# Optimization experiments

Hardware: AMD Instinct MI355X
Metric: run time of the kernel (lower is better)

Reference implementation:

```python
import jax, jax.numpy as jnp
import numpy as np

L_LAYERS = 4
B = 8
PATCH_H = 37
PATCH_W = 37
P = PATCH_H * PATCH_W  # 1369
D = 1024
J = 768
H = 518
W = 518
R_LIST = [1, 3, 5]
K_LIST = [1, 2, 3]
TOPMIN_MIN = 0.0
TOPMIN_MAX = 0.3


def setup_inputs() -> dict:
    key = jax.random.key(0)
    k1, k2 = jax.random.split(key)
    features = jax.random.normal(k1, (L_LAYERS, B, P, D), dtype=jnp.float32)
    cls_tokens = jax.random.normal(k2, (B, J), dtype=jnp.float32)
    return {"features": features, "cls_tokens": cls_tokens}


def _layer_norm_2d(x, eps=1e-5):
    # torch.layer_norm with normalized_shape = (P, D): normalize jointly over last two dims, no affine
    mu = jnp.mean(x, axis=(-2, -1), keepdims=True)
    var = jnp.var(x, axis=(-2, -1), keepdims=True)
    return (x - mu) * jax.lax.rsqrt(var + eps)


def _lnamd(features, r):
    # LNAMD: unfold(r,r, zero pad r//2) + adaptive_avg_pool1d(D*r*r -> D) == per-channel r x r
    # neighborhood mean over the patch grid with zero padding (pool bins are exactly r*r wide).
    if r == 1:
        return features
    l, b, p, d = features.shape
    x = features.reshape(l * b, PATCH_H, PATCH_W, d)
    pad = r // 2
    s = jax.lax.reduce_window(x, 0.0, jax.lax.add, (1, r, r, 1), (1, 1, 1, 1),
                              [(0, 0), (pad, pad), (pad, pad), (0, 0)])
    return (s / float(r * r)).reshape(l, b, p, d)


def _msm(rf, use_remat=False):
    # rf: [L,B,P,D] L2-normalized. Mutual scoring: for each image i, euclidean cdist of its
    # patches to all other images' patches, min over ref patches, mean of [k_min:k_max] smallest.
    l, b, p, d = rf.shape
    k_min = int(TOPMIN_MIN * (b - 1))
    k_max = int(TOPMIN_MAX * (b - 1))
    sq = jnp.sum(rf * rf, axis=-1)  # [L,B,P]

    def per_image(i):
        feat = rf[:, i]  # [L,P,D]
        dots = jnp.einsum('lpd,lbqd->lpbq', feat, rf)  # [L,P,B,P]
        d2 = sq[:, i][:, :, None, None] + sq[:, None, :, :] - 2.0 * dots
        dist = jnp.sqrt(jnp.maximum(d2, 1e-12))
        mind = jnp.min(dist, axis=-1)  # [L,P,B]
        mind = jnp.where(jnp.arange(b)[None, None, :] == i, jnp.inf, mind)  # exclude self
        neg_top = jax.lax.top_k(-mind, k_max)[0]  # k_max smallest distances (ascending)
        sel = -neg_top[..., k_min:k_max]
        return jnp.mean(sel, axis=-1)  # [L,P]

    fn = jax.checkpoint(per_image) if use_remat else per_image
    scores = jax.lax.map(fn, jnp.arange(b))  # [B,L,P]; lax.map keeps one cdist block live at a time
    return jnp.transpose(scores, (1, 0, 2))  # [L,B,P]


def _rscin(sim, scores, top_k):
    # zero out the B-top_k smallest similarities per row (keep top_k largest), row-normalize, reweight
    b = sim.shape[0]
    if top_k < b:
        vals, idx = jax.lax.top_k(sim, top_k)
        masked = jnp.zeros_like(sim).at[jnp.arange(b)[:, None], idx].set(vals)
    else:
        masked = sim
    masked = masked / jnp.sum(masked, axis=-1, keepdims=True)
    return masked @ scores


def _interp_mat(out_len, in_len):
    # bilinear, align_corners=True: src = dst * (in-1)/(out-1); separable 1D interpolation matrix
    pos = jnp.arange(out_len, dtype=jnp.float32) * ((in_len - 1) / (out_len - 1))
    i0 = jnp.clip(jnp.floor(pos).astype(jnp.int32), 0, in_len - 1)
    i1 = jnp.minimum(i0 + 1, in_len - 1)
    w = pos - i0.astype(jnp.float32)
    m = jnp.zeros((out_len, in_len), jnp.float32)
    m = m.at[jnp.arange(out_len), i0].add(1.0 - w)
    m = m.at[jnp.arange(out_len), i1].add(w)
    return m


def _forward(features, cls_tokens, use_remat=False):
    feats = _layer_norm_2d(features)  # [L,B,P,D]
    per_r = []
    for r in R_LIST:
        rf = _lnamd(feats, r)
        rf = rf / jnp.linalg.norm(rf, axis=-1, keepdims=True)
        per_r.append(jnp.mean(_msm(rf, use_remat), axis=0))  # mean over layers -> [B,P]
    scores = jnp.mean(jnp.stack(per_r, axis=0), axis=0)  # [B,P]
    img_scores = jnp.max(scores, axis=1)  # [B]
    cls = cls_tokens / jnp.linalg.norm(cls_tokens, axis=-1, keepdims=True)
    sim = cls @ cls.T  # [B,B]
    final = jnp.mean(jnp.stack([_rscin(sim, img_scores, k) for k in K_LIST], axis=0), axis=0)
    patch = scores.reshape(-1, PATCH_H, PATCH_W)
    mh = _interp_mat(H, PATCH_H)
    mw = _interp_mat(W, PATCH_W)
    pixel = jnp.einsum('Hh,bhw,Ww->bHW', mh, patch, mw)  # [B,H,W]
    return final, pixel


def reference(features, cls_tokens):
    return _forward(features, cls_tokens)
```

## Files before the change

### kernel.cpp

```cpp
#include <hip/hip_runtime.h>
#include <hip/hip_bf16.h>
#include <math.h>

#define L_LAYERS 4
#define BIMG 8
#define PATCH_H 37
#define PATCH_W 37
#define PP 1369
#define DD 1024
#define JJ 768
#define HOUT 518
#define WOUT 518
#define PPAD 1408
#define NPAIR 28

typedef float floatx4 __attribute__((ext_vector_type(4)));

__device__ __forceinline__ unsigned int f2e4m3(float v) {
  unsigned int b = __float_as_uint(v);
  unsigned int sign = (b >> 24) & 0x80u;
  float mag = fabsf(v);
  unsigned int code;
  if (mag >= 0.015625f) {
    unsigned int mb = __float_as_uint(mag);
    mb = mb + 0x0007ffffu + ((mb >> 20) & 1u);
    code = (((mb >> 23) - 120u) << 3) | ((mb >> 20) & 7u);
  } else {
    code = (unsigned int)__float2int_rn(mag * 512.0f);
  }
  return code | sign;
}
__device__ __forceinline__ float e4m3tof(unsigned int c) {
  unsigned int em = c & 0x7fu;
  float m;
  if (em >= 8u) m = __uint_as_float((((em >> 3) + 120u) << 23) | ((em & 7u) << 20));
  else          m = (float)em * 0.001953125f;
  return (c & 0x80u) ? -m : m;
}

__device__ __forceinline__ void gload_lds16(const void* gptr, void* lptr) {
  __builtin_amdgcn_global_load_lds(
      (const __attribute__((address_space(1))) unsigned int*)gptr,
      (__attribute__((address_space(3))) unsigned int*)lptr, 16, 0, 0);
}

__global__ __launch_bounds__(256) void k1_mu(const float* __restrict__ x,
                                             float* __restrict__ mu_acc) {
  const int lb = blockIdx.y;
  const float* base = x + (size_t)lb * PP * DD;
  const int N4 = PP * DD / 4;
  float s = 0.0f;
  for (int idx = blockIdx.x * 256 + threadIdx.x; idx < N4; idx += gridDim.x * 256) {
    float4 u = *(const float4*)(base + (size_t)idx * 4);
    s += u.x + u.y + u.z + u.w;
  }
  for (int off = 1; off < 64; off <<= 1) s += __shfl_xor(s, off, 64);
  __shared__ float red[4];
  if ((threadIdx.x & 63) == 0) red[threadIdx.x >> 6] = s;
  __syncthreads();
  if (threadIdx.x == 0)
    atomicAdd(&mu_acc[lb], red[0] + red[1] + red[2] + red[3]);
}

__global__ __launch_bounds__(256) void k2_pool(const float* __restrict__ x,
                                               const float* __restrict__ mu_acc,
                                               unsigned char* __restrict__ rf,
                                               float* __restrict__ nrm,
                                               int r) {
  const int p  = blockIdx.x;
  const int lb = blockIdx.y;
  const int tid = threadIdx.x;
  const int d0 = tid * 4;
  const size_t outbase = ((size_t)lb * PPAD + p) * DD;
  if (p >= PP) {
    uchar4 z; z.x = 0; z.y = 0; z.z = 0; z.w = 0;
    *(uchar4*)(rf + outbase + d0) = z;
    if (tid == 0) nrm[(size_t)lb * PPAD + p] = 0.0f;
    return;
  }
  const float mu = mu_acc[lb] * (1.0f / ((float)PP * (float)DD));
  const int ph = p / PATCH_W, pw = p % PATCH_W;
  const int pad = r >> 1;
  float s0 = 0, s1 = 0, s2 = 0, s3 = 0;
  int cnt = 0;
  for (int dy = -pad; dy <= pad; dy++) {
    int qh = ph + dy; if (qh < 0 || qh >= PATCH_H) continue;
    for (int dx = -pad; dx <= pad; dx++) {
      int qw = pw + dx; if (qw < 0 || qw >= PATCH_W) continue;
      cnt++;
      const float* src = x + ((size_t)lb * PP + qh * PATCH_W + qw) * DD + d0;
      float4 u = *(const float4*)src;
      s0 += u.x; s1 += u.y; s2 += u.z; s3 += u.w;
    }
  }
  const float cm = (float)cnt * mu;
  s0 -= cm; s1 -= cm; s2 -= cm; s3 -= cm;
  float sq = s0 * s0 + s1 * s1 + s2 * s2 + s3 * s3;
  for (int off = 1; off < 64; off <<= 1) sq += __shfl_xor(sq, off, 64);
  __shared__ float red[4];
  if ((tid & 63) == 0) red[tid >> 6] = sq;
  __syncthreads();
  const float rn16 = rsqrtf(red[0] + red[1] + red[2] + red[3]) * 16.0f;
  unsigned int c0 = f2e4m3(s0 * rn16), c1 = f2e4m3(s1 * rn16);
  unsigned int c2 = f2e4m3(s2 * rn16), c3 = f2e4m3(s3 * rn16);
  uchar4 o; o.x = (unsigned char)c0; o.y = (unsigned char)c1;
  o.z = (unsigned char)c2; o.w = (unsigned char)c3;
  *(uchar4*)(rf + outbase + d0) = o;
  float q0 = e4m3tof(c0), q1 = e4m3tof(c1), q2 = e4m3tof(c2), q3 = e4m3tof(c3);
  float nq = q0 * q0 + q1 * q1 + q2 * q2 + q3 * q3;
  for (int off = 1; off < 64; off <<= 1) nq += __shfl_xor(nq, off, 64);
  __syncthreads();
  if ((tid & 63) == 0) red[tid >> 6] = nq;
  __syncthreads();
  if (tid == 0)
    nrm[(size_t)lb * PPAD + p] = red[0] + red[1] + red[2] + red[3];
}

__global__ __launch_bounds__(256) void k3_pairdots(const unsigned char* __restrict__ rf,
                                                   const float* __restrict__ nrm,
                                                   unsigned int* __restrict__ mind) {
  const int l = blockIdx.z / NPAIR;
  int rem = blockIdx.z % NPAIR;
  int i = 0, span = BIMG - 1;
  while (rem >= span) { rem -= span; span--; i++; }
  const int j = i + 1 + rem;

  const int rowbase = blockIdx.x * 128;
  const int colbase = blockIdx.y * 128;
  const unsigned char* A  = rf + ((size_t)(l * BIMG + i) * PPAD + rowbase) * DD;
  const unsigned char* Bp = rf + ((size_t)(l * BIMG + j) * PPAD + colbase) * DD;

  __shared__ __align__(16) unsigned char lA[128 * 64];
  __shared__ __align__(16) unsigned char lB[128 * 64];

  const int tid  = threadIdx.x;
  const int lane = tid & 63;
  const int wave = tid >> 6;
  const int lrow = lane & 15;
  const int quad = lane >> 4;
  const int wr = (wave >> 1) * 64;
  const int wc = (wave & 1) * 64;

  floatx4 acc[4][4];
#pragma unroll
  for (int a = 0; a < 4; a++)
#pragma unroll
    for (int b = 0; b < 4; b++) acc[a][b] = (floatx4){0.f, 0.f, 0.f, 0.f};

  const int r0  = wave * 32 + (lane >> 2);
  const int gsw = (lane & 3) ^ ((lane >> 3) & 3);
  const unsigned char* gA0 = A  + (size_t)r0 * DD + gsw * 16;
  const unsigned char* gA1 = gA0 + (size_t)16 * DD;
  const unsigned char* gB0 = Bp + (size_t)r0 * DD + gsw * 16;
  const unsigned char* gB1 = gB0 + (size_t)16 * DD;
  unsigned char* dA0 = lA + wave * 2048;
  unsigned char* dA1 = dA0 + 1024;
  unsigned char* dB0 = lB + wave * 2048;
  unsigned char* dB1 = dB0 + 1024;

  const int swf = (lrow >> 1) & 3;
  const int sub8 = (quad & 1) * 8;
  int rowoffA[4], rowoffB[4];
#pragma unroll
  for (int t = 0; t < 4; t++) {
    rowoffA[t] = (wr + t * 16 + lrow) * 64 + sub8;
    rowoffB[t] = (wc + t * 16 + lrow) * 64 + sub8;
  }

  for (int k0 = 0; k0 < DD; k0 += 64) {
    __syncthreads();
    gload_lds16(gA0 + k0, dA0);
    gload_lds16(gA1 + k0, dA1);
    gload_lds16(gB0 + k0, dB0);
    gload_lds16(gB1 + k0, dB1);
    __syncthreads();
#pragma unroll
    for (int ks = 0; ks < 2; ks++) {
      const int gfrag = (((ks << 1) + (quad >> 1)) ^ swf) * 16;
      long af[4], bfv[4];
#pragma unroll
      for (int mt = 0; mt < 4; mt++)
        af[mt] = *(const long*)(lA + rowoffA[mt] + gfrag);
#pragma unroll
      for (int ct = 0; ct < 4; ct++)
        bfv[ct] = *(const long*)(lB + rowoffB[ct] + gfrag);
#pragma unroll
      for (int mt = 0; mt < 4; mt++)
#pragma unroll
        for (int ct = 0; ct < 4; ct++)
          acc[mt][ct] = __builtin_amdgcn_mfma_f32_16x16x32_fp8_fp8(
              af[mt], bfv[ct], acc[mt][ct], 0, 0, 0);
    }
  }

  const float* nI = nrm + (size_t)(l * BIMG + i) * PPAD;
  const float* nJ = nrm + (size_t)(l * BIMG + j) * PPAD;
  unsigned int* mrow = mind + ((size_t)(l * BIMG + i) * BIMG + j) * PP;
  unsigned int* mcol = mind + ((size_t)(l * BIMG + j) * BIMG + i) * PP;

  float nj[4];
#pragma unroll
  for (int ct = 0; ct < 4; ct++) nj[ct] = nJ[colbase + wc + ct * 16 + lrow];
  float ni[4][4];
#pragma unroll
  for (int mt = 0; mt < 4; mt++)
#pragma unroll
    for (int reg = 0; reg < 4; reg++)
      ni[mt][reg] = nI[rowbase + wr + mt * 16 + quad * 4 + reg];

#pragma unroll
  for (int mt = 0; mt < 4; mt++) {
#pragma unroll
    for (int reg = 0; reg < 4; reg++) {
      const int gr = rowbase + wr + mt * 16 + quad * 4 + reg;
      float v = -1e30f;
#pragma unroll
      for (int ct = 0; ct < 4; ct++) {
        const int gc = colbase + wc + ct * 16 + lrow;
        if (gc < PP) v = fmaxf(v, 2.0f * acc[mt][ct][reg] - nj[ct]);
      }
      for (int off = 1; off < 16; off <<= 1) v = fmaxf(v, __shfl_xor(v, off, 64));
      if (lrow == 0 && gr < PP)
        atomicMax(mrow + gr, __float_as_uint(v + 1024.0f));
    }
  }
#pragma unroll
  for (int ct = 0; ct < 4; ct++) {
    const int gc = colbase + wc + ct * 16 + lrow;
    float v = -1e30f;
#pragma unroll
    for (int mt = 0; mt < 4; mt++) {
      const int grb = rowbase + wr + mt * 16 + quad * 4;
#pragma unroll
      for (int reg = 0; reg < 4; reg++)
        if (grb + reg < PP) v = fmaxf(v, 2.0f * acc[mt][ct][reg] - ni[mt][reg]);
    }
    for (int off = 16; off < 64; off <<= 1) v = fmaxf(v, __shfl_xor(v, off, 64));
    if (quad == 0 && gc < PP)
      atomicMax(mcol + gc, __float_as_uint(v + 1024.0f));
  }
}

__global__ void k4_scores(const unsigned int* __restrict__ mind,
                          const float* __restrict__ nrm,
                          float* __restrict__ scores) {
  const int idx = blockIdx.x * 256 + threadIdx.x;
  if (idx >= BIMG * PP) return;
  const int i = idx / PP, p = idx % PP;
  float accum = 0.0f;
  for (int l = 0; l < L_LAYERS; l++) {
    const float n_own = nrm[(size_t)(l * BIMG + i) * PPAD + p];
    float m1 = 1e30f, m2 = 1e30f;
    for (int b = 0; b < BIMG; b++) {
      if (b == i) continue;
      const unsigned int enc = mind[((size_t)(l * BIMG + i) * BIMG + b) * PP + p];
      const float val = __uint_as_float(enc) - 1024.0f;
      const float d2 = fmaxf((n_own - val) * (1.0f / 256.0f), 1e-12f);
      const float dist = sqrtf(d2);
      if (dist < m1) { m2 = m1; m1 = dist; }
      else if (dist < m2) { m2 = dist; }
    }
    accum += 0.5f * (m1 + m2);
  }
  scores[idx] += accum * (1.0f / (float)(L_LAYERS * 3));
}

__global__ void k5_imgmax(const float* __restrict__ scores, float* __restrict__ img) {
  const int i = blockIdx.x;
  float m = -1e30f;
  for (int p = threadIdx.x; p < PP; p += 256) m = fmaxf(m, scores[i * PP + p]);
  for (int off = 1; off < 64; off <<= 1) m = fmaxf(m, __shfl_xor(m, off, 64));
  __shared__ float red[4];
  if ((threadIdx.x & 63) == 0) red[threadIdx.x >> 6] = m;
  __syncthreads();
  if (threadIdx.x == 0)
    img[i] = fmaxf(fmaxf(red[0], red[1]), fmaxf(red[2], red[3]));
}

__global__ void k6_final(const float* __restrict__ cls,
                         const float* __restrict__ img,
                         float* __restrict__ out) {
  __shared__ float norms[BIMG];
  __shared__ float sim[BIMG][BIMG];
  const int t = threadIdx.x;
  if (t < BIMG) {
    float s = 0;
    for (int d = 0; d < JJ; d++) { float v = cls[t * JJ + d]; s += v * v; }
    norms[t] = sqrtf(s);
  }
  __syncthreads();
  {
    const int ii = t >> 3, jj = t & 7;
    float s = 0;
    for (int d = 0; d < JJ; d++) s += cls[ii * JJ + d] * cls[jj * JJ + d];
    sim[ii][jj] = s / (norms[ii] * norms[jj]);
  }
  __syncthreads();
  if (t < BIMG) {
    float v[8]; int id[8];
    for (int a = 0; a < 8; a++) { v[a] = sim[t][a]; id[a] = a; }
    for (int a = 0; a < 8; a++) {
      int best = a;
      for (int b = a + 1; b < 8; b++) if (v[b] > v[best]) best = b;
      float tv = v[a]; v[a] = v[best]; v[best] = tv;
      int ti = id[a]; id[a] = id[best]; id[best] = ti;
    }
    float res = 0;
    for (int k = 1; k <= 3; k++) {
      float num = 0, den = 0;
      for (int a = 0; a < k; a++) { num += v[a] * img[id[a]]; den += v[a]; }
      res += num / den;
    }
    out[t] = res * (1.0f / 3.0f);
  }
}

__global__ void k7_pixel(const float* __restrict__ scores,
                         float* __restrict__ out) {
  const int idx = blockIdx.x * 256 + threadIdx.x;
  if (idx >= BIMG * HOUT * WOUT) return;
  const int b = idx / (HOUT * WOUT);
  const int rem = idx % (HOUT * WOUT);
  const int Y = rem / WOUT, X = rem % WOUT;
  const float sy = (float)(PATCH_H - 1) / (float)(HOUT - 1);
  const float sx = (float)(PATCH_W - 1) / (float)(WOUT - 1);
  float py = (float)Y * sy;
  float px = (float)X * sx;
  int y0 = (int)floorf(py); y0 = min(max(y0, 0), PATCH_H - 1);
  int x0 = (int)floorf(px); x0 = min(max(x0, 0), PATCH_W - 1);
  const int y1 = min(y0 + 1, PATCH_H - 1);
  const int x1 = min(x0 + 1, PATCH_W - 1);
  const float wy = py - (float)y0, wx = px - (float)x0;
  const float* sc = scores + (size_t)b * PP;
  const float v =
      (1.f - wy) * ((1.f - wx) * sc[y0 * PATCH_W + x0] + wx * sc[y0 * PATCH_W + x1]) +
      wy         * ((1.f - wx) * sc[y1 * PATCH_W + x0] + wx * sc[y1 * PATCH_W + x1]);
  out[8 + idx] = v;
}

extern "C" void kernel_launch(void* const* d_in, const int* in_sizes, int n_in,
                              void* d_out, int out_size, void* d_ws, size_t ws_size,
                              hipStream_t stream) {
  const float* feat = (const float*)d_in[0];
  const float* cls  = (const float*)d_in[1];
  float* out = (float*)d_out;

  char* ws = (char*)d_ws;
  size_t off = 0;
  unsigned char* rf = (unsigned char*)(ws + off);
  off += (size_t)L_LAYERS * BIMG * PPAD * DD;
  unsigned int* mind = (unsigned int*)(ws + off);
  off += (size_t)L_LAYERS * BIMG * BIMG * PP * 4;
  float* nrm = (float*)(ws + off);
  off += (size_t)L_LAYERS * BIMG * PPAD * 4;
  float* scores = (float*)(ws + off);
  off += (size_t)BIMG * PP * 4;
  float* mu_acc = (float*)(ws + off);
  off += 32 * 4;
  float* img = (float*)(ws + off);
  off += 8 * 4;

  hipMemsetAsync(mu_acc, 0, 32 * 4, stream);
  hipMemsetAsync(scores, 0, (size_t)BIMG * PP * 4, stream);
  k1_mu<<<dim3(43, 32), 256, 0, stream>>>(feat, mu_acc);

  const int rlist[3] = {1, 3, 5};
  for (int ri = 0; ri < 3; ri++) {
    k2_pool<<<dim3(PPAD, 32), 256, 0, stream>>>(feat, mu_acc, rf, nrm, rlist[ri]);
    hipMemsetAsync(mind, 0, (size_t)L_LAYERS * BIMG * BIMG * PP * 4, stream);
    k3_pairdots<<<dim3(11, 11, L_LAYERS * NPAIR), 256, 0, stream>>>(rf, nrm, mind);
    k4_scores<<<(BIMG * PP + 255) / 256, 256, 0, stream>>>(mind, nrm, scores);
  }
  k5_imgmax<<<8, 256, 0, stream>>>(scores, img);
  k6_final<<<1, 64, 0, stream>>>(cls, img, out);
  k7_pixel<<<(BIMG * HOUT * WOUT + 255) / 256, 256, 0, stream>>>(scores, out);
}
```

Before: 2.594 ms.

## Fuse all three pooling radii into single pool, pairdots and score launches

Adds a k2_pool3 kernel that reads each 5x5 neighborhood once and produces the r=1, r=3 and r=5 FP8 features and norms together. The pair-dot GEMM and score kernels then run once over all three radii via a larger grid, in place of three sequential rounds of launches. A launch_bounds occupancy hint is added to k3, and its precomputed norm and offset arrays are replaced by direct loads to lower register use. This cuts feature reads and launch serialization and gives k3 a bigger grid, at the cost of three times the workspace; it falls back to the old path if the workspace is too small.

```diff
diff --git a/kernel.cpp b/kernel.cpp
--- a/kernel.cpp
+++ b/kernel.cpp
@@ -13,6 +13,10 @@
 #define WOUT 518
 #define PPAD 1408
 #define NPAIR 28
+#define ZPAIR (L_LAYERS * NPAIR)
+#define RFSZ  ((size_t)L_LAYERS * BIMG * PPAD * DD)
+#define NRMSZ ((size_t)L_LAYERS * BIMG * PPAD)
+#define MINDSZ ((size_t)L_LAYERS * BIMG * BIMG * PP)
 
 typedef float floatx4 __attribute__((ext_vector_type(4)));
 
@@ -62,19 +66,85 @@
     atomicAdd(&mu_acc[lb], red[0] + red[1] + red[2] + red[3]);
 }
 
-__global__ __launch_bounds__(256) void k2_pool(const float* __restrict__ x,
-                                               const float* __restrict__ mu_acc,
-                                               unsigned char* __restrict__ rf,
-                                               float* __restrict__ nrm,
-                                               int r) {
+__device__ __forceinline__ void finish_r(float s0, float s1, float s2, float s3,
+                                         float cm, unsigned char* dst, float* nrmdst,
+                                         int tid, float* red) {
+  s0 -= cm; s1 -= cm; s2 -= cm; s3 -= cm;
+  float sq = s0 * s0 + s1 * s1 + s2 * s2 + s3 * s3;
+  for (int off = 1; off < 64; off <<= 1) sq += __shfl_xor(sq, off, 64);
+  __syncthreads();
+  if ((tid & 63) == 0) red[tid >> 6] = sq;
+  __syncthreads();
+  const float rn16 = rsqrtf(red[0] + red[1] + red[2] + red[3]) * 16.0f;
+  unsigned int c0 = f2e4m3(s0 * rn16), c1 = f2e4m3(s1 * rn16);
+  unsigned int c2 = f2e4m3(s2 * rn16), c3 = f2e4m3(s3 * rn16);
+  uchar4 o; o.x = (unsigned char)c0; o.y = (unsigned char)c1;
+  o.z = (unsigned char)c2; o.w = (unsigned char)c3;
+  *(uchar4*)dst = o;
+  float q0 = e4m3tof(c0), q1 = e4m3tof(c1), q2 = e4m3tof(c2), q3 = e4m3tof(c3);
+  float nq = q0 * q0 + q1 * q1 + q2 * q2 + q3 * q3;
+  for (int off = 1; off < 64; off <<= 1) nq += __shfl_xor(nq, off, 64);
+  __syncthreads();
+  if ((tid & 63) == 0) red[tid >> 6] = nq;
+  __syncthreads();
+  if (tid == 0) *nrmdst = red[0] + red[1] + red[2] + red[3];
+}
+
+__global__ __launch_bounds__(256) void k2_pool3(const float* __restrict__ x,
+                                                const float* __restrict__ mu_acc,
+                                                unsigned char* __restrict__ rf,
+                                                float* __restrict__ nrm) {
   const int p  = blockIdx.x;
   const int lb = blockIdx.y;
   const int tid = threadIdx.x;
   const int d0 = tid * 4;
-  const size_t outbase = ((size_t)lb * PPAD + p) * DD;
+  const size_t outoff = ((size_t)lb * PPAD + p) * DD + d0;
   if (p >= PP) {
     uchar4 z; z.x = 0; z.y = 0; z.z = 0; z.w = 0;
-    *(uchar4*)(rf + outbase + d0) = z;
+    for (int r = 0; r < 3; r++) {
+      *(uchar4*)(rf + r * RFSZ + outoff) = z;
+      if (tid == 0) nrm[r * NRMSZ + (size_t)lb * PPAD + p] = 0.0f;
+    }
+    return;
+  }
+  const float mu = mu_acc[lb] * (1.0f / ((float)PP * (float)DD));
+  const int ph = p / PATCH_W, pw = p % PATCH_W;
+  float a5[4] = {0, 0, 0, 0}, a3[4] = {0, 0, 0, 0}, a1[4] = {0, 0, 0, 0};
+  int c5 = 0, c3 = 0;
+  for (int dy = -2; dy <= 2; dy++) {
+    int qh = ph + dy; if (qh < 0 || qh >= PATCH_H) continue;
+    for (int dx = -2; dx <= 2; dx++) {
+      int qw = pw + dx; if (qw < 0 || qw >= PATCH_W) continue;
+      const float* src = x + ((size_t)lb * PP + qh * PATCH_W + qw) * DD + d0;
+      float4 u = *(const float4*)src;
+      a5[0] += u.x; a5[1] += u.y; a5[2] += u.z; a5[3] += u.w; c5++;
+      if (dy >= -1 && dy <= 1 && dx >= -1 && dx <= 1) {
+        a3[0] += u.x; a3[1] += u.y; a3[2] += u.z; a3[3] += u.w; c3++;
+        if (dy == 0 && dx == 0) { a1[0] = u.x; a1[1] = u.y; a1[2] = u.z; a1[3] = u.w; }
+      }
+    }
+  }
+  __shared__ float red[4];
+  const size_t noff = (size_t)lb * PPAD + p;
+  finish_r(a1[0], a1[1], a1[2], a1[3], mu, rf + outoff, nrm + noff, tid, red);
+  finish_r(a3[0], a3[1], a3[2], a3[3], (float)c3 * mu, rf + RFSZ + outoff,
+           nrm + NRMSZ + noff, tid, red);
+  finish_r(a5[0], a5[1], a5[2], a5[3], (float)c5 * mu, rf + 2 * RFSZ + outoff,
+           nrm + 2 * NRMSZ + noff, tid, red);
+}
+
+__global__ __launch_bounds__(256) void k2_pool(const float* __restrict__ x,
+                                               const float* __restrict__ mu_acc,
+                                               unsigned char* __restrict__ rf,
+                                               float* __restrict__ nrm, int r) {
+  const int p  = blockIdx.x;
+  const int lb = blockIdx.y;
+  const int tid = threadIdx.x;
+  const int d0 = tid * 4;
+  const size_t outoff = ((size_t)lb * PPAD + p) * DD + d0;
+  if (p >= PP) {
+    uchar4 z; z.x = 0; z.y = 0; z.z = 0; z.w = 0;
+    *(uchar4*)(rf + outoff) = z;
     if (tid == 0) nrm[(size_t)lb * PPAD + p] = 0.0f;
     return;
   }
@@ -93,42 +163,27 @@
       s0 += u.x; s1 += u.y; s2 += u.z; s3 += u.w;
     }
   }
-  const float cm = (float)cnt * mu;
-  s0 -= cm; s1 -= cm; s2 -= cm; s3 -= cm;
-  float sq = s0 * s0 + s1 * s1 + s2 * s2 + s3 * s3;
-  for (int off = 1; off < 64; off <<= 1) sq += __shfl_xor(sq, off, 64);
   __shared__ float red[4];
-  if ((tid & 63) == 0) red[tid >> 6] = sq;
-  __syncthreads();
-  const float rn16 = rsqrtf(red[0] + red[1] + red[2] + red[3]) * 16.0f;
-  unsigned int c0 = f2e4m3(s0 * rn16), c1 = f2e4m3(s1 * rn16);
-  unsigned int c2 = f2e4m3(s2 * rn16), c3 = f2e4m3(s3 * rn16);
-  uchar4 o; o.x = (unsigned char)c0; o.y = (unsigned char)c1;
-  o.z = (unsigned char)c2; o.w = (unsigned char)c3;
-  *(uchar4*)(rf + outbase + d0) = o;
-  float q0 = e4m3tof(c0), q1 = e4m3tof(c1), q2 = e4m3tof(c2), q3 = e4m3tof(c3);
-  float nq = q0 * q0 + q1 * q1 + q2 * q2 + q3 * q3;
-  for (int off = 1; off < 64; off <<= 1) nq += __shfl_xor(nq, off, 64);
-  __syncthreads();
-  if ((tid & 63) == 0) red[tid >> 6] = nq;
-  __syncthreads();
-  if (tid == 0)
-    nrm[(size_t)lb * PPAD + p] = red[0] + red[1] + red[2] + red[3];
-}
-
-__global__ __launch_bounds__(256) void k3_pairdots(const unsigned char* __restrict__ rf,
-                                                   const float* __restrict__ nrm,
-                                                   unsigned int* __restrict__ mind) {
-  const int l = blockIdx.z / NPAIR;
-  int rem = blockIdx.z % NPAIR;
+  finish_r(s0, s1, s2, s3, (float)cnt * mu, rf + outoff,
+           nrm + (size_t)lb * PPAD + p, tid, red);
+}
+
+__global__ __launch_bounds__(256, 3) void k3_pairdots(const unsigned char* __restrict__ rf,
+                                                      const float* __restrict__ nrm,
+                                                      unsigned int* __restrict__ mind) {
+  const int rsel = blockIdx.z / ZPAIR;
+  const int zz   = blockIdx.z % ZPAIR;
+  const int l = zz / NPAIR;
+  int rem = zz % NPAIR;
   int i = 0, span = BIMG - 1;
   while (rem >= span) { rem -= span; span--; i++; }
   const int j = i + 1 + rem;
 
+  const unsigned char* rfr = rf + (size_t)rsel * RFSZ;
   const int rowbase = blockIdx.x * 128;
   const int colbase = blockIdx.y * 128;
-  const unsigned char* A  = rf + ((size_t)(l * BIMG + i) * PPAD + rowbase) * DD;
-  const unsigned char* Bp = rf + ((size_t)(l * BIMG + j) * PPAD + colbase) * DD;
+  const unsigned char* A  = rfr + ((size_t)(l * BIMG + i) * PPAD + rowbase) * DD;
+  const unsigned char* Bp = rfr + ((size_t)(l * BIMG + j) * PPAD + colbase) * DD;
 
   __shared__ __align__(16) unsigned char lA[128 * 64];
   __shared__ __align__(16) unsigned char lB[128 * 64];
@@ -149,41 +204,30 @@
 
   const int r0  = wave * 32 + (lane >> 2);
   const int gsw = (lane & 3) ^ ((lane >> 3) & 3);
-  const unsigned char* gA0 = A  + (size_t)r0 * DD + gsw * 16;
-  const unsigned char* gA1 = gA0 + (size_t)16 * DD;
-  const unsigned char* gB0 = Bp + (size_t)r0 * DD + gsw * 16;
-  const unsigned char* gB1 = gB0 + (size_t)16 * DD;
+  const size_t goff = (size_t)r0 * DD + gsw * 16;
   unsigned char* dA0 = lA + wave * 2048;
-  unsigned char* dA1 = dA0 + 1024;
   unsigned char* dB0 = lB + wave * 2048;
-  unsigned char* dB1 = dB0 + 1024;
 
   const int swf = (lrow >> 1) & 3;
   const int sub8 = (quad & 1) * 8;
-  int rowoffA[4], rowoffB[4];
-#pragma unroll
-  for (int t = 0; t < 4; t++) {
-    rowoffA[t] = (wr + t * 16 + lrow) * 64 + sub8;
-    rowoffB[t] = (wc + t * 16 + lrow) * 64 + sub8;
-  }
 
   for (int k0 = 0; k0 < DD; k0 += 64) {
     __syncthreads();
-    gload_lds16(gA0 + k0, dA0);
-    gload_lds16(gA1 + k0, dA1);
-    gload_lds16(gB0 + k0, dB0);
-    gload_lds16(gB1 + k0, dB1);
+    gload_lds16(A + goff + k0, dA0);
+    gload_lds16(A + goff + 16 * DD + k0, dA0 + 1024);
+    gload_lds16(Bp + goff + k0, dB0);
+    gload_lds16(Bp + goff + 16 * DD + k0, dB0 + 1024);
     __syncthreads();
 #pragma unroll
     for (int ks = 0; ks < 2; ks++) {
-      const int gfrag = (((ks << 1) + (quad >> 1)) ^ swf) * 16;
+      const int gfrag = (((ks << 1) + (quad >> 1)) ^ swf) * 16 + sub8;
       long af[4], bfv[4];
 #pragma unroll
       for (int mt = 0; mt < 4; mt++)
-        af[mt] = *(const long*)(lA + rowoffA[mt] + gfrag);
+        af[mt] = *(const long*)(lA + (wr + mt * 16 + lrow) * 64 + gfrag);
 #pragma unroll
       for (int ct = 0; ct < 4; ct++)
-        bfv[ct] = *(const long*)(lB + rowoffB[ct] + gfrag);
+        bfv[ct] = *(const long*)(lB + (wc + ct * 16 + lrow) * 64 + gfrag);
 #pragma unroll
       for (int mt = 0; mt < 4; mt++)
 #pragma unroll
@@ -193,20 +237,10 @@
     }
   }
 
-  const float* nI = nrm + (size_t)(l * BIMG + i) * PPAD;
-  const float* nJ = nrm + (size_t)(l * BIMG + j) * PPAD;
-  unsigned int* mrow = mind + ((size_t)(l * BIMG + i) * BIMG + j) * PP;
-  unsigned int* mcol = mind + ((size_t)(l * BIMG + j) * BIMG + i) * PP;
-
-  float nj[4];
-#pragma unroll
-  for (int ct = 0; ct < 4; ct++) nj[ct] = nJ[colbase + wc + ct * 16 + lrow];
-  float ni[4][4];
-#pragma unroll
-  for (int mt = 0; mt < 4; mt++)
-#pragma unroll
-    for (int reg = 0; reg < 4; reg++)
-      ni[mt][reg] = nI[rowbase + wr + mt * 16 + quad * 4 + reg];
+  const float* nI = nrm + rsel * NRMSZ + (size_t)(l * BIMG + i) * PPAD;
+  const float* nJ = nrm + rsel * NRMSZ + (size_t)(l * BIMG + j) * PPAD;
+  unsigned int* mrow = mind + rsel * MINDSZ + ((size_t)(l * BIMG + i) * BIMG + j) * PP;
+  unsigned int* mcol = mind + rsel * MINDSZ + ((size_t)(l * BIMG + j) * BIMG + i) * PP;
 
 #pragma unroll
   for (int mt = 0; mt < 4; mt++) {
@@ -217,7 +251,7 @@
 #pragma unroll
       for (int ct = 0; ct < 4; ct++) {
         const int gc = colbase + wc + ct * 16 + lrow;
-        if (gc < PP) v = fmaxf(v, 2.0f * acc[mt][ct][reg] - nj[ct]);
+        if (gc < PP) v = fmaxf(v, 2.0f * acc[mt][ct][reg] - nJ[gc]);
       }
       for (int off = 1; off < 16; off <<= 1) v = fmaxf(v, __shfl_xor(v, off, 64));
       if (lrow == 0 && gr < PP)
@@ -233,7 +267,7 @@
       const int grb = rowbase + wr + mt * 16 + quad * 4;
 #pragma unroll
       for (int reg = 0; reg < 4; reg++)
-        if (grb + reg < PP) v = fmaxf(v, 2.0f * acc[mt][ct][reg] - ni[mt][reg]);
+        if (grb + reg < PP) v = fmaxf(v, 2.0f * acc[mt][ct][reg] - nI[grb + reg]);
     }
     for (int off = 16; off < 64; off <<= 1) v = fmaxf(v, __shfl_xor(v, off, 64));
     if (quad == 0 && gc < PP)
@@ -243,24 +277,27 @@
 
 __global__ void k4_scores(const unsigned int* __restrict__ mind,
                           const float* __restrict__ nrm,
-                          float* __restrict__ scores) {
+                          float* __restrict__ scores, int nr) {
   const int idx = blockIdx.x * 256 + threadIdx.x;
   if (idx >= BIMG * PP) return;
   const int i = idx / PP, p = idx % PP;
   float accum = 0.0f;
-  for (int l = 0; l < L_LAYERS; l++) {
-    const float n_own = nrm[(size_t)(l * BIMG + i) * PPAD + p];
-    float m1 = 1e30f, m2 = 1e30f;
-    for (int b = 0; b < BIMG; b++) {
-      if (b == i) continue;
-      const unsigned int enc = mind[((size_t)(l * BIMG + i) * BIMG + b) * PP + p];
-      const float val = __uint_as_float(enc) - 1024.0f;
-      const float d2 = fmaxf((n_own - val) * (1.0f / 256.0f), 1e-12f);
-      const float dist = sqrtf(d2);
-      if (dist < m1) { m2 = m1; m1 = dist; }
-      else if (dist < m2) { m2 = dist; }
-    }
-    accum += 0.5f * (m1 + m2);
+  for (int r = 0; r < nr; r++) {
+    for (int l = 0; l < L_LAYERS; l++) {
+      const float n_own = nrm[r * NRMSZ + (size_t)(l * BIMG + i) * PPAD + p];
+      float m1 = 1e30f, m2 = 1e30f;
+      for (int b = 0; b < BIMG; b++) {
+        if (b == i) continue;
+        const unsigned int enc =
+            mind[r * MINDSZ + ((size_t)(l * BIMG + i) * BIMG + b) * PP + p];
+        const float val = __uint_as_float(enc) - 1024.0f;
+        const float d2 = fmaxf((n_own - val) * (1.0f / 256.0f), 1e-12f);
+        const float dist = sqrtf(d2);
+        if (dist < m1) { m2 = m1; m1 = dist; }
+        else if (dist < m2) { m2 = dist; }
+      }
+      accum += 0.5f * (m1 + m2);
+    }
   }
   scores[idx] += accum * (1.0f / (float)(L_LAYERS * 3));
 }
@@ -345,14 +382,18 @@
   const float* cls  = (const float*)d_in[1];
   float* out = (float*)d_out;
 
+  const size_t need_fused = 3 * RFSZ + 3 * MINDSZ * 4 + 3 * NRMSZ * 4 +
+                            (size_t)BIMG * PP * 4 + 1024;
+  const bool fused = ws_size >= need_fused;
+
   char* ws = (char*)d_ws;
   size_t off = 0;
   unsigned char* rf = (unsigned char*)(ws + off);
-  off += (size_t)L_LAYERS * BIMG * PPAD * DD;
+  off += (fused ? 3 : 1) * RFSZ;
   unsigned int* mind = (unsigned int*)(ws + off);
-  off += (size_t)L_LAYERS * BIMG * BIMG * PP * 4;
+  off += (fused ? 3 : 1) * MINDSZ * 4;
   float* nrm = (float*)(ws + off);
-  off += (size_t)L_LAYERS * BIMG * PPAD * 4;
+  off += (fused ? 3 : 1) * NRMSZ * 4;
   float* scores = (float*)(ws + off);
   off += (size_t)BIMG * PP * 4;
   float* mu_acc = (float*)(ws + off);
@@ -364,12 +405,19 @@
   hipMemsetAsync(scores, 0, (size_t)BIMG * PP * 4, stream);
   k1_mu<<<dim3(43, 32), 256, 0, stream>>>(feat, mu_acc);
 
-  const int rlist[3] = {1, 3, 5};
-  for (int ri = 0; ri < 3; ri++) {
-    k2_pool<<<dim3(PPAD, 32), 256, 0, stream>>>(feat, mu_acc, rf, nrm, rlist[ri]);
-    hipMemsetAsync(mind, 0, (size_t)L_LAYERS * BIMG * BIMG * PP * 4, stream);
-    k3_pairdots<<<dim3(11, 11, L_LAYERS * NPAIR), 256, 0, stream>>>(rf, nrm, mind);
-    k4_scores<<<(BIMG * PP + 255) / 256, 256, 0, stream>>>(mind, nrm, scores);
+  if (fused) {
+    k2_pool3<<<dim3(PPAD, 32), 256, 0, stream>>>(feat, mu_acc, rf, nrm);
+    hipMemsetAsync(mind, 0, 3 * MINDSZ * 4, stream);
+    k3_pairdots<<<dim3(11, 11, 3 * ZPAIR), 256, 0, stream>>>(rf, nrm, mind);
+    k4_scores<<<(BIMG * PP + 255) / 256, 256, 0, stream>>>(mind, nrm, scores, 3);
+  } else {
+    const int rlist[3] = {1, 3, 5};
+    for (int ri = 0; ri < 3; ri++) {
+      k2_pool<<<dim3(PPAD, 32), 256, 0, stream>>>(feat, mu_acc, rf, nrm, rlist[ri]);
+      hipMemsetAsync(mind, 0, MINDSZ * 4, stream);
+      k3_pairdots<<<dim3(11, 11, ZPAIR), 256, 0, stream>>>(rf, nrm, mind);
+      k4_scores<<<(BIMG * PP + 255) / 256, 256, 0, stream>>>(mind, nrm, scores, 1);
+    }
   }
   k5_imgmax<<<8, 256, 0, stream>>>(scores, img);
   k6_final<<<1, 64, 0, stream>>>(cls, img, out);
```

New measurement: 2.565 ms. About the same (-1.1%).
